# Optimization experiments

Measured on AMD Instinct MI355X. Metric: run time of the kernel, lower is better.

## Reference

```python
import jax, jax.numpy as jnp
import numpy as np

E = 512   # decoder embedding dim
H = 2048  # decoder hidden size


def setup_inputs() -> dict:
    key = jax.random.key(0)
    ks = jax.random.split(key, 10)
    V, B, T, S = 50000, 32, 128, 128
    s = 0.05
    return {
        "embed_table": jax.random.normal(ks[0], (V, E), jnp.float32) * s,
        "encoder_outs": jax.random.normal(ks[1], (S, B, 2 * 512), jnp.float32),
        "encoder_hiddens": jax.random.normal(ks[2], (1, B, H), jnp.float32) * s,
        "encoder_cells": jax.random.normal(ks[3], (1, B, H), jnp.float32) * s,
        "W_ih": jax.random.normal(ks[4], (4 * H, 2048), jnp.float32) * s,
        "W_hh": jax.random.normal(ks[5], (4 * H, H), jnp.float32) * s,
        "b_ih": jax.random.normal(ks[6], (4 * H,), jnp.float32) * s,
        "b_hh": jax.random.normal(ks[7], (4 * H,), jnp.float32) * s,
        "prev_output_tokens": jax.random.randint(ks[8], (B, T), 0, V),
        "tgt_langs": jax.random.randint(ks[9], (B,), 0, V),
    }


def reference(embed_table, encoder_outs, encoder_hiddens, encoder_cells,
              W_ih, W_hh, b_ih, b_hh, prev_output_tokens, tgt_langs):
    # bottleneck: max-pool encoder states over source time (LASER-style)
    context = jnp.max(encoder_outs, axis=0)                 # [B, 2*enc_hidden]
    x = embed_table[prev_output_tokens]                      # [B, T, E]
    x = jnp.transpose(x, (1, 0, 2))                          # [T, B, E]
    lang_embed = embed_table[tgt_langs]                      # [B, E]

    # Per-step LSTM input is concat(x_t, lang, context). lang/context are
    # time-invariant, so precompute their gate contribution once.
    static_in = jnp.concatenate([lang_embed, context], axis=1)   # [B, E + 2*enc]
    gates_x = (jnp.einsum('tbe,ge->tbg', x, W_ih[:, :E])
               + static_in @ W_ih[:, E:].T + b_ih + b_hh)        # [T, B, 4H]

    h0 = encoder_hiddens[0]
    c0 = encoder_cells[0]

    def step(carry, g_x):
        h, c = carry
        gates = g_x + h @ W_hh.T                              # [B, 4H]
        i, f, g, o = jnp.split(gates, 4, axis=1)
        c = jax.nn.sigmoid(f) * c + jax.nn.sigmoid(i) * jnp.tanh(g)
        h = jax.nn.sigmoid(o) * jnp.tanh(c)
        return (h, c), h

    _, outs = jax.lax.scan(step, (h0, c0), gates_x)           # [T, B, H]
    return outs
```

## Files before the change

kernel.cpp:

```cpp
#include <hip/hip_runtime.h>
#include <math.h>

#define E_DIM 512
#define H_DIM 2048
#define G_DIM 8192
#define B_DIM 32
#define T_DIM 128
#define S_DIM 128
#define ENC2  1024
#define SI_DIM 1536

#define NBLK 256
#define NTHR 512
#define JT   8
#define KHW  (H_DIM/8)
#define KXW  (E_DIM/8)
#define HB   (B_DIM*H_DIM)
#define HPLANE 65536



typedef __bf16 bf16_t;
typedef bf16_t bf16x8 __attribute__((ext_vector_type(8)));
typedef float f32x4 __attribute__((ext_vector_type(4)));
typedef unsigned int u32x4 __attribute__((ext_vector_type(4)));

__device__ __forceinline__ unsigned short f2bf(float x) {
    unsigned u = __float_as_uint(x);
    u += 0x7FFFu + ((u >> 16) & 1u);
    return (unsigned short)(u >> 16);
}
__device__ __forceinline__ float bf2f(unsigned short s) {
    return __uint_as_float(((unsigned)s) << 16);
}
__device__ __forceinline__ unsigned pack2(float a, float b) {
    return (unsigned)f2bf(a) | ((unsigned)f2bf(b) << 16);
}
__device__ __forceinline__ f32x4 mfma16(bf16x8 a, bf16x8 b, f32x4 c) {
    return __builtin_amdgcn_mfma_f32_16x16x32_bf16(a, b, c, 0, 0, 0);
}
__device__ __forceinline__ bf16x8 tofrag(u32x4 q) {
    return __builtin_bit_cast(bf16x8, q);
}
__device__ __forceinline__ float sigf(float x) { return 1.f / (1.f + expf(-x)); }

#define OPAQUE(v) asm volatile("" : "+v"(v))
#define ALD(p) __hip_atomic_load((p), __ATOMIC_RELAXED, __HIP_MEMORY_SCOPE_AGENT)
#define AST(p, v) __hip_atomic_store((p), (v), __ATOMIC_RELAXED, __HIP_MEMORY_SCOPE_AGENT)

struct WPair { u32x4 hi, lo; };
__device__ __forceinline__ WPair packW(const float* src) {
    float4 w0 = *(const float4*)src;
    float4 w1 = *(const float4*)(src + 16);
    u32x4 qh;
    qh.x = pack2(w0.x, w0.y); qh.y = pack2(w0.z, w0.w);
    qh.z = pack2(w1.x, w1.y); qh.w = pack2(w1.z, w1.w);
    float r0 = w0.x - bf2f((unsigned short)(qh.x & 0xFFFF));
    float r1 = w0.y - bf2f((unsigned short)(qh.x >> 16));
    float r2 = w0.z - bf2f((unsigned short)(qh.y & 0xFFFF));
    float r3 = w0.w - bf2f((unsigned short)(qh.y >> 16));
    float r4 = w1.x - bf2f((unsigned short)(qh.z & 0xFFFF));
    float r5 = w1.y - bf2f((unsigned short)(qh.z >> 16));
    float r6 = w1.z - bf2f((unsigned short)(qh.w & 0xFFFF));
    float r7 = w1.w - bf2f((unsigned short)(qh.w >> 16));
    u32x4 ql;
    ql.x = pack2(r0, r1); ql.y = pack2(r2, r3);
    ql.z = pack2(r4, r5); ql.w = pack2(r6, r7);
    WPair out; out.hi = qh; out.lo = ql;
    return out;
}

__global__ void k_prep(const float* __restrict__ enc_outs, const float* __restrict__ embed,
                       const int* __restrict__ langs, const float* __restrict__ h0,
                       float* __restrict__ si, unsigned short* __restrict__ hth,
                       unsigned short* __restrict__ htl, unsigned int* __restrict__ flags) {
    int tid = blockIdx.x * blockDim.x + threadIdx.x;
    int np = gridDim.x * blockDim.x;
    for (int i = tid; i < NBLK * 16; i += np)
        flags[i] = 0u;
    for (int i = tid; i < B_DIM * ENC2; i += np) {
        int b = i >> 10, e = i & 1023;
        float m = -3.4e38f;
        for (int s = 0; s < S_DIM; ++s)
            m = fmaxf(m, enc_outs[(s * B_DIM + b) * ENC2 + e]);
        si[b * SI_DIM + E_DIM + e] = m;
    }
    for (int i = tid; i < B_DIM * E_DIM; i += np) {
        int b = i >> 9, e = i & 511;
        si[b * SI_DIM + e] = embed[(long)langs[b] * E_DIM + e];
    }
    for (int i = tid; i < B_DIM * H_DIM; i += np) {
        int b = i >> 11, j = i & 2047;
        float h = h0[i];
        unsigned short hi = f2bf(h);
        unsigned short lo = f2bf(h - bf2f(hi));
        int T = j >> 5, lgp = (j & 15) >> 2, o = (j & 3) + 4 * ((j & 31) >> 4);
        int idx = ((T * 4 + lgp) * 32 + b) * 8 + o;
        hth[idx] = hi;
        htl[idx] = lo;
    }
}

__global__ void k_gather_x(const float* __restrict__ embed, const int* __restrict__ tok,
                           unsigned short* __restrict__ xh, unsigned short* __restrict__ xl) {
    int r = blockIdx.x;
    int t = r >> 5, b = r & 31;
    long row = tok[b * T_DIM + t];
    const float4* src = (const float4*)(embed + row * E_DIM);
    unsigned* xhp = (unsigned*)(xh + (size_t)t * 16384);
    unsigned* xlp = (unsigned*)(xl + (size_t)t * 16384);
    for (int g = threadIdx.x; g < 128; g += blockDim.x) {
        float4 v = src[g];
        unsigned h01 = pack2(v.x, v.y), h23 = pack2(v.z, v.w);
        float rx = v.x - bf2f((unsigned short)(h01 & 0xFFFF));
        float ry = v.y - bf2f((unsigned short)(h01 >> 16));
        float rz = v.z - bf2f((unsigned short)(h23 & 0xFFFF));
        float rw = v.w - bf2f((unsigned short)(h23 >> 16));
        int T = g >> 3, lgp = g & 3, o0 = 4 * ((g & 7) >> 2);
        int u32i = ((T * 4 + lgp) * 32 + b) * 4 + (o0 >> 1);
        uint2 qh; qh.x = h01; qh.y = h23;
        uint2 ql; ql.x = pack2(rx, ry); ql.y = pack2(rz, rw);
        *(uint2*)(xhp + u32i) = qh;
        *(uint2*)(xlp + u32i) = ql;
    }
}

#define MFMA12(PH, PL, IT) \
    acc00 = mfma16(Ah0, tofrag(PH##0##IT), acc00); \
    acc00 = mfma16(Ah0, tofrag(PL##0##IT), acc00); \
    acc00 = mfma16(Al0, tofrag(PH##0##IT), acc00); \
    acc01 = mfma16(Ah1, tofrag(PH##0##IT), acc01); \
    acc01 = mfma16(Ah1, tofrag(PL##0##IT), acc01); \
    acc01 = mfma16(Al1, tofrag(PH##0##IT), acc01); \
    acc10 = mfma16(Ah0, tofrag(PH##1##IT), acc10); \
    acc10 = mfma16(Ah0, tofrag(PL##1##IT), acc10); \
    acc10 = mfma16(Al0, tofrag(PH##1##IT), acc10); \
    acc11 = mfma16(Ah1, tofrag(PH##1##IT), acc11); \
    acc11 = mfma16(Ah1, tofrag(PL##1##IT), acc11); \
    acc11 = mfma16(Al1, tofrag(PH##1##IT), acc11);

#define AX_IT(IT) do { \
    const int fb = ((wv * 2 + (IT)) * 4 + lg) * 32 + lr; \
    bf16x8 Ah0 = __builtin_bit_cast(bf16x8, xh4[fb]); \
    bf16x8 Ah1 = __builtin_bit_cast(bf16x8, xh4[fb + 16]); \
    bf16x8 Al0 = __builtin_bit_cast(bf16x8, xl4[fb]); \
    bf16x8 Al1 = __builtin_bit_cast(bf16x8, xl4[fb + 16]); \
    MFMA12(Xh, Xl, IT) \
} while (0)

#define AH_IT(IT) do { \
    const int fb = ((wv * 8 + (IT)) * 4 + lg) * 32 + lr; \
    bf16x8 Ah0 = __builtin_bit_cast(bf16x8, hh4[fb]); \
    bf16x8 Ah1 = __builtin_bit_cast(bf16x8, hh4[fb + 16]); \
    bf16x8 Al0 = __builtin_bit_cast(bf16x8, hl4[fb]); \
    bf16x8 Al1 = __builtin_bit_cast(bf16x8, hl4[fb + 16]); \
    MFMA12(Wh, Wl, IT) \
} while (0)

#define PK_HH(F, IT) { WPair p = packW(W_hh + (long)rowf##F * H_DIM + (wv * KHW + IT * 32 + 4 * lg)); \
                       Wh##F##IT = p.hi; Wl##F##IT = p.lo; }
#define PK_X(F, IT)  { WPair p = packW(W_ih + (long)rowf##F * 2048 + (wv * KXW + IT * 32 + 4 * lg)); \
                       Xh##F##IT = p.hi; Xl##F##IT = p.lo; }

__global__ __launch_bounds__(NTHR, 2) void k_lstm(
        const unsigned short* __restrict__ xh, const unsigned short* __restrict__ xl,
        unsigned short* __restrict__ hth, unsigned short* __restrict__ htl,
        const float* __restrict__ si, const float* __restrict__ W_ih,
        const float* __restrict__ W_hh, const float* __restrict__ b_ih,
        const float* __restrict__ b_hh, const float* __restrict__ c0,
        float* __restrict__ out, unsigned int* __restrict__ flags) {
    __shared__ f32x4 red[8][2][2][64];
    __shared__ float sgl[4][B_DIM][JT];

    const int tid = threadIdx.x;
    const int wv = tid >> 6, l = tid & 63, lr = l & 15, lg = l >> 4;
    const int jb = blockIdx.x * JT;

    {
        int c = tid >> 4, bp = tid & 15;
        int gate = c >> 3, jl = c & 7;
        long grow = (long)(gate * H_DIM + jb + jl);
        const float* wrow = W_ih + grow * 2048 + E_DIM;
        const float* s0 = si + bp * SI_DIM;
        const float* s1 = si + (bp + 16) * SI_DIM;
        float a0 = 0.f, a1 = 0.f;
        for (int k = 0; k < SI_DIM; k += 4) {
            float4 w  = *(const float4*)(wrow + k);
            float4 x0 = *(const float4*)(s0 + k);
            float4 x1 = *(const float4*)(s1 + k);
            a0 += w.x * x0.x + w.y * x0.y + w.z * x0.z + w.w * x0.w;
            a1 += w.x * x1.x + w.y * x1.y + w.z * x1.z + w.w * x1.w;
        }
        float bias = b_ih[grow] + b_hh[grow];
        sgl[gate][bp][jl] = a0 + bias;
        sgl[gate][bp + 16][jl] = a1 + bias;
    }

    const int rowf0 = ((lr >> 3)) * H_DIM + jb + (lr & 7);
    const int rowf1 = (2 + (lr >> 3)) * H_DIM + jb + (lr & 7);

    u32x4 Wh00, Wh01, Wh02, Wh03, Wh04, Wh05, Wh06, Wh07;
    u32x4 Wh10, Wh11, Wh12, Wh13, Wh14, Wh15, Wh16, Wh17;
    u32x4 Wl00, Wl01, Wl02, Wl03, Wl04, Wl05, Wl06, Wl07;
    u32x4 Wl10, Wl11, Wl12, Wl13, Wl14, Wl15, Wl16, Wl17;
    u32x4 Xh00, Xh01, Xh10, Xh11, Xl00, Xl01, Xl10, Xl11;

    PK_HH(0, 0) PK_HH(0, 1) PK_HH(0, 2) PK_HH(0, 3)
    PK_HH(0, 4) PK_HH(0, 5) PK_HH(0, 6) PK_HH(0, 7)
    PK_HH(1, 0) PK_HH(1, 1) PK_HH(1, 2) PK_HH(1, 3)
    PK_HH(1, 4) PK_HH(1, 5) PK_HH(1, 6) PK_HH(1, 7)
    PK_X(0, 0) PK_X(0, 1) PK_X(1, 0) PK_X(1, 1)

    OPAQUE(Wh00); OPAQUE(Wh01); OPAQUE(Wh02); OPAQUE(Wh03);
    OPAQUE(Wh04); OPAQUE(Wh05); OPAQUE(Wh06); OPAQUE(Wh07);
    OPAQUE(Wh10); OPAQUE(Wh11); OPAQUE(Wh12); OPAQUE(Wh13);
    OPAQUE(Wh14); OPAQUE(Wh15); OPAQUE(Wh16); OPAQUE(Wh17);
    OPAQUE(Wl00); OPAQUE(Wl01); OPAQUE(Wl02); OPAQUE(Wl03);
    OPAQUE(Wl04); OPAQUE(Wl05); OPAQUE(Wl06); OPAQUE(Wl07);
    OPAQUE(Wl10); OPAQUE(Wl11); OPAQUE(Wl12); OPAQUE(Wl13);
    OPAQUE(Wl14); OPAQUE(Wl15); OPAQUE(Wl16); OPAQUE(Wl17);
    OPAQUE(Xh00); OPAQUE(Xh01); OPAQUE(Xh10); OPAQUE(Xh11);
    OPAQUE(Xl00); OPAQUE(Xl01); OPAQUE(Xl10); OPAQUE(Xl11);

    const int ab = tid >> 3, ajl = tid & 7;
    float creg = 0.f;
    if (tid < 256) creg = c0[ab * H_DIM + jb + ajl];

    __syncthreads();

    #pragma unroll 1
    for (int t = 0; t < T_DIM; ++t) {
        f32x4 acc00 = {}, acc01 = {}, acc10 = {}, acc11 = {};

        {
            const uint4* xh4 = (const uint4*)(xh + (size_t)t * 16384);
            const uint4* xl4 = (const uint4*)(xl + (size_t)t * 16384);
            AX_IT(0); AX_IT(1);
        }

        if (t > 0) {
            const unsigned tgt = (unsigned)t;
            const unsigned int* fp =
                flags + (size_t)(wv * 32 + (l & 31)) * 16 + (l >> 5);
            for (;;) {
                unsigned v0 = ALD(fp);
                unsigned v1 = ALD(fp + 2);
                if (__all(v0 >= tgt && v1 >= tgt)) break;
                __builtin_amdgcn_s_sleep(1);
            }
            __builtin_amdgcn_sched_barrier(0);
        }

        {
            const uint4* hh4 = (const uint4*)(hth + (size_t)t * HPLANE);
            const uint4* hl4 = (const uint4*)(htl + (size_t)t * HPLANE);
            AH_IT(0); AH_IT(1); AH_IT(2); AH_IT(3);
            AH_IT(4); AH_IT(5); AH_IT(6); AH_IT(7);
        }

        red[wv][0][0][l] = acc00; red[wv][0][1][l] = acc01;
        red[wv][1][0][l] = acc10; red[wv][1][1][l] = acc11;
        __syncthreads();

        float gs[4];
        if (tid < 256) {
            const int m = ab >> 4, r = ab & 3, q = (ab & 15) >> 2;
            #pragma unroll
            for (int g = 0; g < 4; ++g) {
                const int l2 = (q << 4) | ((g & 1) * 8 + ajl);
                float s = 0.f;
                #pragma unroll
                for (int w = 0; w < 8; ++w)
                    s += red[w][g >> 1][m][l2][r];
                gs[g] = s + sgl[g][ab][ajl];
            }
        }
        __syncthreads();

        if (tid < 256) {
            float cn = sigf(gs[1]) * creg + sigf(gs[0]) * tanhf(gs[2]);
            float hn = sigf(gs[3]) * tanhf(cn);
            creg = cn;
            unsigned short hh = f2bf(hn);
            unsigned short hl = f2bf(hn - bf2f(hh));
            unsigned nhh = __shfl_down((unsigned)hh, 1);
            unsigned nhl = __shfl_down((unsigned)hl, 1);
            if ((ajl & 1) == 0) {
                unsigned* hthn = (unsigned*)(hth + (size_t)(t + 1) * HPLANE);
                unsigned* htln = (unsigned*)(htl + (size_t)(t + 1) * HPLANE);
                int j0 = jb + ajl;
                int T = j0 >> 5, lgp = (j0 & 15) >> 2;
                int o = (j0 & 3) + 4 * ((j0 & 31) >> 4);
                int u32i = ((T * 4 + lgp) * 32 + ab) * 4 + (o >> 1);
                AST(hthn + u32i, (unsigned)hh | (nhh << 16));
                AST(htln + u32i, (unsigned)hl | (nhl << 16));
            }
            asm volatile("s_waitcnt vmcnt(0)" ::: "memory");
            if (l == 0 && t < T_DIM - 1)
                AST(flags + (size_t)blockIdx.x * 16 + wv, (unsigned)(t + 1));
            out[(size_t)t * HB + ab * H_DIM + jb + ajl] = hn;
        }
    }
}

extern "C" void kernel_launch(void* const* d_in, const int* in_sizes, int n_in,
                              void* d_out, int out_size, void* d_ws, size_t ws_size,
                              hipStream_t stream) {
    const float* embed    = (const float*)d_in[0];
    const float* enc_outs = (const float*)d_in[1];
    const float* h0       = (const float*)d_in[2];
    const float* c0       = (const float*)d_in[3];
    const float* W_ih     = (const float*)d_in[4];
    const float* W_hh     = (const float*)d_in[5];
    const float* b_ih     = (const float*)d_in[6];
    const float* b_hh     = (const float*)d_in[7];
    const int*   tok      = (const int*)d_in[8];
    const int*   langs    = (const int*)d_in[9];
    float* out = (float*)d_out;

    char* ws = (char*)d_ws;
    unsigned short* xh  = (unsigned short*)(ws + 0);
    unsigned short* xl  = (unsigned short*)(ws + 4194304);
    unsigned short* hth = (unsigned short*)(ws + 8388608);
    unsigned short* htl = (unsigned short*)(ws + 25296896);
    float*          si  = (float*)(ws + 42205184);
    unsigned int* flags = (unsigned int*)(ws + 42401792);

    hipLaunchKernelGGL(k_prep, dim3(512), dim3(256), 0, stream,
                       enc_outs, embed, langs, h0, si, hth, htl, flags);
    hipLaunchKernelGGL(k_gather_x, dim3(T_DIM * B_DIM), dim3(128), 0, stream,
                       embed, tok, xh, xl);
    hipLaunchKernelGGL(k_lstm, dim3(NBLK), dim3(NTHR), 0, stream,
                       xh, xl, hth, htl, si, W_ih, W_hh, b_ih, b_hh, c0,
                       out, flags);
}
```

Baseline: 971.8 us.

## Split flag polling into two phases and double-buffer reduction scratch

```diff
diff --git a/kernel.cpp b/kernel.cpp
--- a/kernel.cpp
+++ b/kernel.cpp
@@ -162,6 +162,18 @@
 #define PK_X(F, IT)  { WPair p = packW(W_ih + (long)rowf##F * 2048 + (wv * KXW + IT * 32 + 4 * lg)); \
                        Xh##F##IT = p.hi; Xl##F##IT = p.lo; }
 
+#define POLL(PH) do { \
+    const unsigned tgt = (unsigned)t; \
+    const unsigned int* fp = \
+        flags + (size_t)(wv * 32 + (PH) * 16 + (l >> 2)) * 16 + (l & 3); \
+    for (;;) { \
+        unsigned v = ALD(fp); \
+        if (__all(v >= tgt)) break; \
+        __builtin_amdgcn_s_sleep(1); \
+    } \
+    __builtin_amdgcn_sched_barrier(0); \
+} while (0)
+
 __global__ __launch_bounds__(NTHR, 2) void k_lstm(
         const unsigned short* __restrict__ xh, const unsigned short* __restrict__ xl,
         unsigned short* __restrict__ hth, unsigned short* __restrict__ htl,
@@ -169,7 +181,7 @@
         const float* __restrict__ W_hh, const float* __restrict__ b_ih,
         const float* __restrict__ b_hh, const float* __restrict__ c0,
         float* __restrict__ out, unsigned int* __restrict__ flags) {
-    __shared__ f32x4 red[8][2][2][64];
+    __shared__ f32x4 red[2][8][2][2][64];
     __shared__ float sgl[4][B_DIM][JT];
 
     const int tid = threadIdx.x;
@@ -238,46 +250,34 @@
             AX_IT(0); AX_IT(1);
         }
 
-        if (t > 0) {
-            const unsigned tgt = (unsigned)t;
-            const unsigned int* fp =
-                flags + (size_t)(wv * 32 + (l & 31)) * 16 + (l >> 5);
-            for (;;) {
-                unsigned v0 = ALD(fp);
-                unsigned v1 = ALD(fp + 2);
-                if (__all(v0 >= tgt && v1 >= tgt)) break;
-                __builtin_amdgcn_s_sleep(1);
-            }
-            __builtin_amdgcn_sched_barrier(0);
+        const uint4* hh4 = (const uint4*)(hth + (size_t)t * HPLANE);
+        const uint4* hl4 = (const uint4*)(htl + (size_t)t * HPLANE);
+
+        if (t > 0) POLL(0);
+        AH_IT(0); AH_IT(1); AH_IT(2); AH_IT(3);
+        if (t > 0) POLL(1);
+        AH_IT(4); AH_IT(5); AH_IT(6); AH_IT(7);
+
+        {
+            f32x4 (*rd)[2][2][64] = red[t & 1];
+            rd[wv][0][0][l] = acc00; rd[wv][0][1][l] = acc01;
+            rd[wv][1][0][l] = acc10; rd[wv][1][1][l] = acc11;
         }
-
-        {
-            const uint4* hh4 = (const uint4*)(hth + (size_t)t * HPLANE);
-            const uint4* hl4 = (const uint4*)(htl + (size_t)t * HPLANE);
-            AH_IT(0); AH_IT(1); AH_IT(2); AH_IT(3);
-            AH_IT(4); AH_IT(5); AH_IT(6); AH_IT(7);
-        }
-
-        red[wv][0][0][l] = acc00; red[wv][0][1][l] = acc01;
-        red[wv][1][0][l] = acc10; red[wv][1][1][l] = acc11;
         __syncthreads();
 
-        float gs[4];
         if (tid < 256) {
+            f32x4 (*rd)[2][2][64] = red[t & 1];
             const int m = ab >> 4, r = ab & 3, q = (ab & 15) >> 2;
+            float gs[4];
             #pragma unroll
             for (int g = 0; g < 4; ++g) {
                 const int l2 = (q << 4) | ((g & 1) * 8 + ajl);
                 float s = 0.f;
                 #pragma unroll
                 for (int w = 0; w < 8; ++w)
-                    s += red[w][g >> 1][m][l2][r];
+                    s += rd[w][g >> 1][m][l2][r];
                 gs[g] = s + sgl[g][ab][ajl];
             }
-        }
-        __syncthreads();
-
-        if (tid < 256) {
             float cn = sigf(gs[1]) * creg + sigf(gs[0]) * tanhf(gs[2]);
             float hn = sigf(gs[3]) * tanhf(cn);
             creg = cn;
```

New measurement: 1.112 ms. 1.14x slower.
